# Kernel optimization log

Measured on AMD Instinct MI355X. Metric: run time of the kernel, lower is better.

Reference implementation:

```python
import jax, jax.numpy as jnp
import numpy as np

B, N, E, D, AD = 8, 1000, 4, 64, 32  # batch, n_node, n_edge_types, state_dim, annotation_dim
W_SCALE = 0.02  # matches normal_(0.0, 0.02) init


def setup_inputs() -> dict:
    key = jax.random.key(0)
    ks = jax.random.split(key, 10)
    return {
        "prop_state": jax.random.normal(ks[0], (B, N, D), jnp.float32),
        "annotation": jax.random.normal(ks[1], (B, N, AD), jnp.float32),
        "A": jax.random.uniform(ks[2], (B, N, 2 * N * E), jnp.float32),
        "W_in": W_SCALE * jax.random.normal(ks[3], (E, D, D), jnp.float32),
        "W_out": W_SCALE * jax.random.normal(ks[4], (E, D, D), jnp.float32),
        "W_r": W_SCALE * jax.random.normal(ks[5], (D, 3 * D), jnp.float32),
        "W_z": W_SCALE * jax.random.normal(ks[6], (D, 3 * D), jnp.float32),
        "W_h": W_SCALE * jax.random.normal(ks[7], (D, 3 * D), jnp.float32),
        "Wo1": W_SCALE * jax.random.normal(ks[8], (D, D + AD), jnp.float32),
        "Wo2": W_SCALE * jax.random.normal(ks[9], (1, D), jnp.float32),
    }


def _propagate(state, A_in, A_out, W_in, W_out, W_r, W_z, W_h):
    b, n, d = state.shape
    e = W_in.shape[0]
    # per-edge-type linear transforms (torch Linear: y = x @ W.T), batched over edge types
    # layout matches torch: stack over e then transpose(0,1) -> [b, e, n, d] -> [b, e*n, d]
    s_in = jnp.einsum('bnd,efd->benf', state, W_in).reshape(b, e * n, d)
    s_out = jnp.einsum('bnd,efd->benf', state, W_out).reshape(b, e * n, d)
    a_in = jnp.matmul(A_in, s_in)    # [b, n, d]
    a_out = jnp.matmul(A_out, s_out)  # [b, n, d]
    a = jnp.concatenate([a_in, a_out, state], axis=2)  # [b, n, 3d]
    r = jax.nn.sigmoid(a @ W_r.T)
    z = jax.nn.sigmoid(a @ W_z.T)
    joined = jnp.concatenate([a_in, a_out, r * state], axis=2)
    h_hat = jnp.tanh(joined @ W_h.T)
    return (1.0 - z) * state + z * h_hat


def reference(prop_state, annotation, A, W_in, W_out, W_r, W_z, W_h, Wo1, Wo2):
    n = prop_state.shape[1]
    e = W_in.shape[0]
    ne = n * e
    A_in, A_out = A[:, :, :ne], A[:, :, ne:]
    # exactly two propagation steps (n_steps_flag path in the original)
    s1 = _propagate(prop_state, A_in, A_out, W_in, W_out, W_r, W_z, W_h)
    s2 = _propagate(s1, A_in, A_out, W_in, W_out, W_r, W_z, W_h)
    join_state = jnp.concatenate([s2, annotation], axis=2)  # [b, n, d+ad]
    out = jnp.tanh(join_state @ Wo1.T) @ Wo2.T  # [b, n, 1]
    return out.sum(axis=2)  # [b, n]
```

## Files before the change

kernel.cpp:

```cpp
#include <hip/hip_runtime.h>


typedef float  f32x4_t  __attribute__((ext_vector_type(4)));
typedef __bf16 bf16x8_t __attribute__((ext_vector_type(8)));
typedef __bf16 bf16x4_t __attribute__((ext_vector_type(4)));

#define MFMA16(a, b, c) __builtin_amdgcn_mfma_f32_16x16x32_bf16((a), (b), (c), 0, 0, 0)

static constexpr int kN     = 1000;
static constexpr int kD     = 64;
static constexpr int kAD    = 32;
static constexpr int kP     = 8000 * 64;
static constexpr int kPl    = 5;

__device__ __forceinline__ float4 ld4(const float* p) {
    return *reinterpret_cast<const float4*>(p);
}

__device__ __forceinline__ bf16x8_t cvt8(float4 a, float4 b) {
    bf16x8_t r;
    r[0] = (__bf16)a.x; r[1] = (__bf16)a.y; r[2] = (__bf16)a.z; r[3] = (__bf16)a.w;
    r[4] = (__bf16)b.x; r[5] = (__bf16)b.y; r[6] = (__bf16)b.z; r[7] = (__bf16)b.w;
    return r;
}

__device__ __forceinline__ bf16x8_t sum5p(const float* p) {
    float s0 = 0.f, s1 = 0.f, s2 = 0.f, s3 = 0.f;
    float s4 = 0.f, s5 = 0.f, s6 = 0.f, s7 = 0.f;
    #pragma unroll
    for (int pl = 0; pl < kPl; ++pl) {
        const float4 a0 = ld4(p + (size_t)pl * kP);
        const float4 a1 = ld4(p + (size_t)pl * kP + 4);
        s0 += a0.x; s1 += a0.y; s2 += a0.z; s3 += a0.w;
        s4 += a1.x; s5 += a1.y; s6 += a1.z; s7 += a1.w;
    }
    bf16x8_t r;
    r[0] = (__bf16)s0; r[1] = (__bf16)s1; r[2] = (__bf16)s2; r[3] = (__bf16)s3;
    r[4] = (__bf16)s4; r[5] = (__bf16)s5; r[6] = (__bf16)s6; r[7] = (__bf16)s7;
    return r;
}

__device__ __forceinline__ float sigm(float x) {
    x = fminf(fmaxf(x, -30.f), 30.f);
    return 1.0f / (1.0f + __expf(-x));
}

__device__ __forceinline__ float fast_tanh(float x) {
    x = fminf(fmaxf(x, -15.f), 15.f);
    const float e = __expf(-2.0f * x);
    return (1.0f - e) / (1.0f + e);
}

__global__ __launch_bounds__(256) void precompute_swt(
    const float* __restrict__ state,
    const float* __restrict__ W_in,
    const float* __restrict__ W_out,
    __bf16* __restrict__ SWTfrag)
{
    const int bx = blockIdx.x;
    const int jt = bx & 15;
    const int e  = (bx >> 4) & 3;
    const int h  = (bx >> 6) & 1;
    const int b  = bx >> 7;
    const float* W = (h ? W_out : W_in) + e * kD * kD;

    const int tid  = threadIdx.x;
    const int w    = tid >> 6;
    const int lane = tid & 63;
    const int m    = lane & 15;
    const int q    = lane >> 4;

    __shared__ __bf16 T[64][72];

    const int  jj    = jt * 64 + w * 16 + m;
    const bool valid = (jj < kN);
    const float* srow = state + ((size_t)b * kN + (valid ? jj : kN - 1)) * kD + q * 8;
    float4 a0 = ld4(srow),      a1 = ld4(srow + 4);
    float4 a2 = ld4(srow + 32), a3 = ld4(srow + 36);
    if (!valid) {
        a0 = make_float4(0.f, 0.f, 0.f, 0.f); a1 = a0; a2 = a0; a3 = a0;
    }
    const bf16x8_t af0 = cvt8(a0, a1);
    const bf16x8_t af1 = cvt8(a2, a3);

    #pragma unroll
    for (int c = 0; c < 4; ++c) {
        const int f = c * 16 + m;
        const float* wrow = W + f * kD + q * 8;
        const bf16x8_t bf0 = cvt8(ld4(wrow),      ld4(wrow + 4));
        const bf16x8_t bf1 = cvt8(ld4(wrow + 32), ld4(wrow + 36));
        f32x4_t acc = {0.f, 0.f, 0.f, 0.f};
        acc = MFMA16(af0, bf0, acc);
        acc = MFMA16(af1, bf1, acc);
        const int j0 = w * 16 + q * 4;
        bf16x4_t v;
        v[0] = (__bf16)acc[0]; v[1] = (__bf16)acc[1];
        v[2] = (__bf16)acc[2]; v[3] = (__bf16)acc[3];
        *reinterpret_cast<bf16x4_t*>(&T[f][j0]) = v;
    }
    __syncthreads();

    const int bh = b * 2 + h;
    #pragma unroll
    for (int rep = 0; rep < 2; ++rep) {
        const int m2 = tid & 15;
        const int cc = (tid >> 4) & 3;
        const int ol = (tid >> 6) + rep * 4;
        const int j0 = jt * 64 + ol * 8;
        if (j0 < kN) {
            const int jg = e * kN + j0;
            const int s  = jg >> 5;
            const int qq = (jg >> 3) & 3;
            const uint4 v = *reinterpret_cast<uint4*>(&T[cc * 16 + m2][ol * 8]);
            const size_t el = ((((size_t)bh * 125 + s) * 4 + cc) * 64 + qq * 16 + m2) * 8;
            *reinterpret_cast<uint4*>((__bf16*)SWTfrag + el) = v;
        }
    }
}

__global__ __launch_bounds__(256, 4) void fused_mm1(
    const float* __restrict__ A,
    const __bf16* __restrict__ SWTfrag,
    __bf16* __restrict__ Afrag,
    float* __restrict__ a_in_p,
    float* __restrict__ a_out_p)
{
    const int bx   = blockIdx.x;
    const int tile = bx & 15;
    const int rest = bx >> 4;
    const int kseg = rest % 5;
    const int rhb  = rest / 5;
    const int h    = rhb & 1;
    const int b    = rhb >> 1;

    const int t    = threadIdx.x;
    const int wv   = t >> 6;
    const int lane = t & 63;
    const int m    = lane & 15;
    const int q    = lane >> 4;

    __shared__ __bf16 L[64][136];

    const float* Abase = A + (size_t)b * kN * 8000 + h * 4000;
    const int bh = b * 2 + h;

    f32x4_t acc0 = {0.f, 0.f, 0.f, 0.f};
    f32x4_t acc1 = {0.f, 0.f, 0.f, 0.f};
    f32x4_t acc2 = {0.f, 0.f, 0.f, 0.f};
    f32x4_t acc3 = {0.f, 0.f, 0.f, 0.f};

    const __bf16* pBbase = SWTfrag + (size_t)bh * 125 * 2048 + (size_t)lane * 8;
    __bf16* pAout = Afrag +
        ((((size_t)(bh * 64 + tile * 4 + wv)) * 125) * 64 + lane) * 8;

    for (int kc = 0; kc < 800; kc += 128) {
        const int cw   = (kc < 768) ? 128 : 32;
        const int kabs = kseg * 800 + kc;
        if (cw == 128) {
            #pragma unroll
            for (int p = 0; p < 4; ++p) {
                const int idx = p * 256 + t;
                const int r   = idx >> 4;
                const int c8  = idx & 15;
                int i = tile * 64 + r;
                if (i >= kN) i = kN - 1;
                const float* src = Abase + (size_t)i * 8000 + kabs + c8 * 8;
                *reinterpret_cast<bf16x8_t*>(&L[r][c8 * 8]) =
                    cvt8(ld4(src), ld4(src + 4));
            }
        } else {
            const int r  = t >> 2;
            const int c8 = t & 3;
            int i = tile * 64 + r;
            if (i >= kN) i = kN - 1;
            const float* src = Abase + (size_t)i * 8000 + kabs + c8 * 8;
            *reinterpret_cast<bf16x8_t*>(&L[r][c8 * 8]) =
                cvt8(ld4(src), ld4(src + 4));
        }
        __syncthreads();
        const int nst = cw >> 5;
        for (int sp = 0; sp < nst; ++sp) {
            const int s = kseg * 25 + (kc >> 5) + sp;
            const bf16x8_t af =
                *reinterpret_cast<const bf16x8_t*>(&L[wv * 16 + m][sp * 32 + q * 8]);
            *reinterpret_cast<bf16x8_t*>(pAout + (size_t)s * 512) = af;

            const __bf16* pB = pBbase + (size_t)s * 2048;
            const bf16x8_t b0 = *(const bf16x8_t*)(pB);
            const bf16x8_t b1 = *(const bf16x8_t*)(pB + 512);
            const bf16x8_t b2 = *(const bf16x8_t*)(pB + 1024);
            const bf16x8_t b3 = *(const bf16x8_t*)(pB + 1536);
            acc0 = MFMA16(af, b0, acc0);
            acc1 = MFMA16(af, b1, acc1);
            acc2 = MFMA16(af, b2, acc2);
            acc3 = MFMA16(af, b3, acc3);
        }
        __syncthreads();
    }

    float* dst = (h ? a_out_p : a_in_p) + (size_t)kseg * kP + (size_t)b * kN * kD;
    const int i0 = tile * 64 + wv * 16 + q * 4;
    #pragma unroll
    for (int r = 0; r < 4; ++r) {
        const int i = i0 + r;
        if (i < kN) {
            float* drow = dst + (size_t)i * kD + m;
            drow[0]  = acc0[r];
            drow[16] = acc1[r];
            drow[32] = acc2[r];
            drow[48] = acc3[r];
        }
    }
}

__global__ __launch_bounds__(256, 4) void big_mm_f(
    const __bf16* __restrict__ Afrag,
    const __bf16* __restrict__ SWTfrag,
    float* __restrict__ a_in_p,
    float* __restrict__ a_out_p)
{
    const int bx   = blockIdx.x;
    const int tile = bx & 15;
    const int h    = (bx >> 4) & 1;
    const int b    = (bx >> 5) & 7;
    const int ksp  = bx >> 8;
    const int t    = threadIdx.x;
    const int wv   = t >> 6;
    const int lane = t & 63;
    const int m    = lane & 15;
    const int q    = lane >> 4;

    const int s0 = ksp * 25;
    const int ns = 25;

    const int bh = b * 2 + h;
    const __bf16* pA = Afrag +
        ((((size_t)(bh * 64 + tile * 4 + wv)) * 125 + s0) * 64 + lane) * 8;
    const __bf16* pB = SWTfrag +
        (((size_t)bh * 125 + s0) * 4 * 64) * 8 + (size_t)lane * 8;

    f32x4_t acc0 = {0.f, 0.f, 0.f, 0.f};
    f32x4_t acc1 = {0.f, 0.f, 0.f, 0.f};
    f32x4_t acc2 = {0.f, 0.f, 0.f, 0.f};
    f32x4_t acc3 = {0.f, 0.f, 0.f, 0.f};

    bf16x8_t cA  = *(const bf16x8_t*)(pA);
    bf16x8_t cB0 = *(const bf16x8_t*)(pB);
    bf16x8_t cB1 = *(const bf16x8_t*)(pB + 512);
    bf16x8_t cB2 = *(const bf16x8_t*)(pB + 1024);
    bf16x8_t cB3 = *(const bf16x8_t*)(pB + 1536);

    for (int s = 0; s < ns; ++s) {
        const int adv = (s + 1 < ns) ? 1 : 0;
        pA += adv * 512;
        pB += adv * 2048;
        const bf16x8_t nA  = *(const bf16x8_t*)(pA);
        const bf16x8_t nB0 = *(const bf16x8_t*)(pB);
        const bf16x8_t nB1 = *(const bf16x8_t*)(pB + 512);
        const bf16x8_t nB2 = *(const bf16x8_t*)(pB + 1024);
        const bf16x8_t nB3 = *(const bf16x8_t*)(pB + 1536);

        acc0 = MFMA16(cA, cB0, acc0);
        acc1 = MFMA16(cA, cB1, acc1);
        acc2 = MFMA16(cA, cB2, acc2);
        acc3 = MFMA16(cA, cB3, acc3);

        cA = nA; cB0 = nB0; cB1 = nB1; cB2 = nB2; cB3 = nB3;
    }

    float* dst = (h ? a_out_p : a_in_p) + (size_t)ksp * kP + (size_t)b * kN * kD;
    const int i0 = tile * 64 + wv * 16 + q * 4;
    #pragma unroll
    for (int r = 0; r < 4; ++r) {
        const int i = i0 + r;
        if (i < kN) {
            float* drow = dst + (size_t)i * kD + m;
            drow[0]  = acc0[r];
            drow[16] = acc1[r];
            drow[32] = acc2[r];
            drow[48] = acc3[r];
        }
    }
}

__global__ __launch_bounds__(256, 2) void gating(
    const float* __restrict__ a_in_p,
    const float* __restrict__ a_out_p,
    const float* __restrict__ state,
    const float* __restrict__ W_r,
    const float* __restrict__ W_z,
    const float* __restrict__ W_h,
    float* __restrict__ s_next,
    const float* __restrict__ ann,
    const float* __restrict__ Wo1,
    const float* __restrict__ Wo2,
    float* __restrict__ out,
    const int step)
{
    const int i0   = blockIdx.x * 16;
    const int tid  = threadIdx.x;
    const int c    = tid >> 6;
    const int lane = tid & 63;
    const int m    = lane & 15;
    const int q    = lane >> 4;
    const int f    = c * 16 + m;

    __shared__ __bf16 TL[16][72];
    __shared__ float  Osum[4][16];

    const size_t rowA = (size_t)(i0 + m);

    bf16x8_t xf[6];
    {
        const float* p = a_in_p + rowA * kD + q * 8;
        xf[0] = sum5p(p);
        xf[1] = sum5p(p + 32);
        p = a_out_p + rowA * kD + q * 8;
        xf[2] = sum5p(p);
        xf[3] = sum5p(p + 32);
        p = state + rowA * kD + q * 8;
        xf[4] = cvt8(ld4(p),      ld4(p + 4));
        xf[5] = cvt8(ld4(p + 32), ld4(p + 36));
    }

    f32x4_t accr = {0.f, 0.f, 0.f, 0.f};
    f32x4_t accz = {0.f, 0.f, 0.f, 0.f};
    f32x4_t acch = {0.f, 0.f, 0.f, 0.f};

    const float* wr = W_r + f * 192 + q * 8;
    const float* wz = W_z + f * 192 + q * 8;
    const float* wh = W_h + f * 192 + q * 8;
    #pragma unroll
    for (int kc = 0; kc < 6; ++kc) {
        accr = MFMA16(xf[kc], cvt8(ld4(wr + kc * 32), ld4(wr + kc * 32 + 4)), accr);
        accz = MFMA16(xf[kc], cvt8(ld4(wz + kc * 32), ld4(wz + kc * 32 + 4)), accz);
        if (kc < 4)
            acch = MFMA16(xf[kc], cvt8(ld4(wh + kc * 32), ld4(wh + kc * 32 + 4)), acch);
    }

    float sC[4];
    #pragma unroll
    for (int r = 0; r < 4; ++r)
        sC[r] = state[(size_t)(i0 + q * 4 + r) * kD + f];

    #pragma unroll
    for (int r = 0; r < 4; ++r)
        TL[q * 4 + r][f] = (__bf16)(sigm(accr[r]) * sC[r]);
    __syncthreads();
    const bf16x8_t rs0 = *(const bf16x8_t*)&TL[m][q * 8];
    const bf16x8_t rs1 = *(const bf16x8_t*)&TL[m][32 + q * 8];

    const float* wh3 = W_h + f * 192 + 128 + q * 8;
    acch = MFMA16(rs0, cvt8(ld4(wh3),      ld4(wh3 + 4)),  acch);
    acch = MFMA16(rs1, cvt8(ld4(wh3 + 32), ld4(wh3 + 36)), acch);

    float ns[4];
    #pragma unroll
    for (int r = 0; r < 4; ++r) {
        const float zv = sigm(accz[r]);
        ns[r] = (1.f - zv) * sC[r] + zv * fast_tanh(acch[r]);
    }

    if (step == 1) {
        #pragma unroll
        for (int r = 0; r < 4; ++r)
            s_next[(size_t)(i0 + q * 4 + r) * kD + f] = ns[r];
    } else {
        __syncthreads();
        #pragma unroll
        for (int r = 0; r < 4; ++r)
            TL[q * 4 + r][f] = (__bf16)ns[r];
        __syncthreads();
        const bf16x8_t j0 = *(const bf16x8_t*)&TL[m][q * 8];
        const bf16x8_t j1 = *(const bf16x8_t*)&TL[m][32 + q * 8];
        const float* ap = ann + rowA * kAD + q * 8;
        const bf16x8_t j2 = cvt8(ld4(ap), ld4(ap + 4));

        f32x4_t acco = {0.f, 0.f, 0.f, 0.f};
        const float* wo = Wo1 + (size_t)f * 96 + q * 8;
        acco = MFMA16(j0, cvt8(ld4(wo),      ld4(wo + 4)),  acco);
        acco = MFMA16(j1, cvt8(ld4(wo + 32), ld4(wo + 36)), acco);
        acco = MFMA16(j2, cvt8(ld4(wo + 64), ld4(wo + 68)), acco);

        const float w2 = Wo2[f];
        float vs[4];
        #pragma unroll
        for (int r = 0; r < 4; ++r)
            vs[r] = fast_tanh(acco[r]) * w2;
        #pragma unroll
        for (int off = 1; off <= 8; off <<= 1) {
            #pragma unroll
            for (int r = 0; r < 4; ++r)
                vs[r] += __shfl_xor(vs[r], off, 64);
        }
        if (m == 0) {
            #pragma unroll
            for (int r = 0; r < 4; ++r)
                Osum[c][q * 4 + r] = vs[r];
        }
        __syncthreads();
        if (tid < 16)
            out[i0 + tid] = Osum[0][tid] + Osum[1][tid] + Osum[2][tid] + Osum[3][tid];
    }
}

extern "C" void kernel_launch(void* const* d_in, const int* in_sizes, int n_in,
                              void* d_out, int out_size, void* d_ws, size_t ws_size,
                              hipStream_t stream) {
    (void)in_sizes; (void)n_in; (void)out_size; (void)ws_size;

    const float* prop_state = (const float*)d_in[0];
    const float* annotation = (const float*)d_in[1];
    const float* A          = (const float*)d_in[2];
    const float* W_in       = (const float*)d_in[3];
    const float* W_out      = (const float*)d_in[4];
    const float* W_r        = (const float*)d_in[5];
    const float* W_z        = (const float*)d_in[6];
    const float* W_h        = (const float*)d_in[7];
    const float* Wo1        = (const float*)d_in[8];
    const float* Wo2        = (const float*)d_in[9];
    float* out = (float*)d_out;

    char* ws = (char*)d_ws;
    __bf16* Afrag   = (__bf16*)(ws);
    __bf16* SWTfrag = (__bf16*)(ws + 131072000);
    float*  a_in_p  = (float*)(ws + 139264000);
    float*  a_out_p = (float*)(ws + 149504000);
    float*  s1      = (float*)(ws + 159744000);

    precompute_swt<<<1024, 256, 0, stream>>>(prop_state, W_in, W_out, SWTfrag);
    fused_mm1<<<1280, 256, 0, stream>>>(A, SWTfrag, Afrag, a_in_p, a_out_p);
    gating<<<500, 256, 0, stream>>>(a_in_p, a_out_p, prop_state, W_r, W_z, W_h,
                                    s1, nullptr, nullptr, nullptr, nullptr, 1);
    precompute_swt<<<1024, 256, 0, stream>>>(s1, W_in, W_out, SWTfrag);
    big_mm_f<<<1280, 256, 0, stream>>>(Afrag, SWTfrag, a_in_p, a_out_p);
    gating<<<500, 256, 0, stream>>>(a_in_p, a_out_p, s1, W_r, W_z, W_h,
                                    nullptr, annotation, Wo1, Wo2, out, 2);
}
```

Baseline: 498.0 us.

## Double-buffer LDS tiles with register prefetch in A-streaming matmul kernel

Restructures the A-tile loop so the global loads for the next chunk are issued into registers before computing the current chunk, with two LDS buffers alternating. This hides global-load latency behind MFMA work and cuts barriers from two per chunk to one. It costs extra registers for the prefetched float4s and doubles the LDS tile, which could reduce occupancy.

```diff
diff --git a/kernel.cpp b/kernel.cpp
--- a/kernel.cpp
+++ b/kernel.cpp
@@ -139,7 +139,7 @@
     const int m    = lane & 15;
     const int q    = lane >> 4;
 
-    __shared__ __bf16 L[64][136];
+    __shared__ __bf16 L[2][64][136];
 
     const float* Abase = A + (size_t)b * kN * 8000 + h * 4000;
     const int bh = b * 2 + h;
@@ -153,50 +153,72 @@
     __bf16* pAout = Afrag +
         ((((size_t)(bh * 64 + tile * 4 + wv)) * 125) * 64 + lane) * 8;
 
-    for (int kc = 0; kc < 800; kc += 128) {
-        const int cw   = (kc < 768) ? 128 : 32;
-        const int kabs = kseg * 800 + kc;
-        if (cw == 128) {
-            #pragma unroll
-            for (int p = 0; p < 4; ++p) {
+    float4 ra[4][2];
+
+    auto load_chunk = [&](int c, bool tail) {
+        const int kabs = kseg * 800 + c * 128;
+        #pragma unroll
+        for (int p = 0; p < 4; ++p) {
+            if (p == 0 || !tail) {
                 const int idx = p * 256 + t;
-                const int r   = idx >> 4;
-                const int c8  = idx & 15;
+                const int r   = tail ? (t >> 2) : (idx >> 4);
+                const int c8  = tail ? (t & 3)  : (idx & 15);
                 int i = tile * 64 + r;
                 if (i >= kN) i = kN - 1;
                 const float* src = Abase + (size_t)i * 8000 + kabs + c8 * 8;
-                *reinterpret_cast<bf16x8_t*>(&L[r][c8 * 8]) =
-                    cvt8(ld4(src), ld4(src + 4));
+                ra[p][0] = ld4(src);
+                ra[p][1] = ld4(src + 4);
             }
-        } else {
-            const int r  = t >> 2;
-            const int c8 = t & 3;
-            int i = tile * 64 + r;
-            if (i >= kN) i = kN - 1;
-            const float* src = Abase + (size_t)i * 8000 + kabs + c8 * 8;
-            *reinterpret_cast<bf16x8_t*>(&L[r][c8 * 8]) =
-                cvt8(ld4(src), ld4(src + 4));
-        }
+        }
+    };
+    auto write_chunk = [&](int buf, bool tail) {
+        #pragma unroll
+        for (int p = 0; p < 4; ++p) {
+            if (p == 0 || !tail) {
+                const int idx = p * 256 + t;
+                const int r   = tail ? (t >> 2) : (idx >> 4);
+                const int c8  = tail ? (t & 3)  : (idx & 15);
+                *reinterpret_cast<bf16x8_t*>(&L[buf][r][c8 * 8]) =
+                    cvt8(ra[p][0], ra[p][1]);
+            }
+        }
+    };
+    auto compute_chunk = [&](int c, int nst, int buf) {
+        #pragma unroll
+        for (int sp = 0; sp < 4; ++sp) {
+            if (sp < nst) {
+                const int s = kseg * 25 + c * 4 + sp;
+                const bf16x8_t af =
+                    *reinterpret_cast<const bf16x8_t*>(&L[buf][wv * 16 + m][sp * 32 + q * 8]);
+                *reinterpret_cast<bf16x8_t*>(pAout + (size_t)s * 512) = af;
+
+                const __bf16* pB = pBbase + (size_t)s * 2048;
+                const bf16x8_t b0 = *(const bf16x8_t*)(pB);
+                const bf16x8_t b1 = *(const bf16x8_t*)(pB + 512);
+                const bf16x8_t b2 = *(const bf16x8_t*)(pB + 1024);
+                const bf16x8_t b3 = *(const bf16x8_t*)(pB + 1536);
+                acc0 = MFMA16(af, b0, acc0);
+                acc1 = MFMA16(af, b1, acc1);
+                acc2 = MFMA16(af, b2, acc2);
+                acc3 = MFMA16(af, b3, acc3);
+            }
+        }
+    };
+
+    load_chunk(0, false);
+    write_chunk(0, false);
+    __syncthreads();
+    load_chunk(1, false);
+
+    #pragma unroll 1
+    for (int c = 0; c < 6; ++c) {
+        compute_chunk(c, 4, c & 1);
+        write_chunk((c + 1) & 1, c + 1 == 6);
         __syncthreads();
-        const int nst = cw >> 5;
-        for (int sp = 0; sp < nst; ++sp) {
-            const int s = kseg * 25 + (kc >> 5) + sp;
-            const bf16x8_t af =
-                *reinterpret_cast<const bf16x8_t*>(&L[wv * 16 + m][sp * 32 + q * 8]);
-            *reinterpret_cast<bf16x8_t*>(pAout + (size_t)s * 512) = af;
-
-            const __bf16* pB = pBbase + (size_t)s * 2048;
-            const bf16x8_t b0 = *(const bf16x8_t*)(pB);
-            const bf16x8_t b1 = *(const bf16x8_t*)(pB + 512);
-            const bf16x8_t b2 = *(const bf16x8_t*)(pB + 1024);
-            const bf16x8_t b3 = *(const bf16x8_t*)(pB + 1536);
-            acc0 = MFMA16(af, b0, acc0);
-            acc1 = MFMA16(af, b1, acc1);
-            acc2 = MFMA16(af, b2, acc2);
-            acc3 = MFMA16(af, b3, acc3);
-        }
-        __syncthreads();
-    }
+        if (c < 5)
+            load_chunk(c + 2, c + 2 == 6);
+    }
+    compute_chunk(6, 1, 0);
 
     float* dst = (h ? a_out_p : a_in_p) + (size_t)kseg * kP + (size_t)b * kN * kD;
     const int i0 = tile * 64 + wv * 16 + q * 4;
```

Measured after the change: 495.7 us. No clear change (-0.5%).
